# Kernel optimization log

Measured on AMD Instinct MI355X. Metric: run time of the kernel, lower is better.

The kernel has to match this reference:

```python
import jax, jax.numpy as jnp
import numpy as np

R = 200000
PAD = 14            # residue_pad_length (atom14)
ACD, ATD, RCD, RID = 32, 8, 32, 32
N_ATOM_CODES, N_ATOM_TYPES, N_RES_CODES = 38, 6, 21
MAX_SEQ = 1024
OUT_0E, OUT_1E = 128, 32
IN0 = PAD * ACD + PAD * ATD + RCD + RID  # 624 scalar (0e) input channels


def setup_inputs() -> dict:
    key = jax.random.key(0)
    ks = jax.random.split(key, 12)
    counts_np = (4 + (np.arange(R) % 11)).astype(np.int32)  # atoms per residue in [4,14]
    n_atoms = int(counts_np.sum())  # 1,799,991
    residue_index_atomwise = jnp.asarray(np.repeat(np.arange(R, dtype=np.int32), counts_np))
    return {
        "relative_coords": jax.random.normal(ks[0], (n_atoms, 3), dtype=jnp.float32),
        "atom_code_index": jax.random.randint(ks[1], (n_atoms,), 1, N_ATOM_CODES, dtype=jnp.int32),
        "atom_type_index": jax.random.randint(ks[2], (n_atoms,), 1, N_ATOM_TYPES, dtype=jnp.int32),
        "residue_index_atomwise": residue_index_atomwise,
        "counts": jnp.asarray(counts_np),
        "residue_code_index": jax.random.randint(ks[3], (R,), 1, N_RES_CODES, dtype=jnp.int32),
        "residue_sequence_index": jax.random.randint(ks[4], (R,), 0, MAX_SEQ, dtype=jnp.int32),
        "base_coords": jax.random.normal(ks[5], (R, 3), dtype=jnp.float32),
        "atom_code_table": jax.random.normal(ks[6], (N_ATOM_CODES, ACD), dtype=jnp.float32),
        "atom_type_table": jax.random.normal(ks[7], (N_ATOM_TYPES, ATD), dtype=jnp.float32),
        "residue_code_table": jax.random.normal(ks[8], (N_RES_CODES, RCD), dtype=jnp.float32),
        "residue_index_table": jax.random.normal(ks[9], (MAX_SEQ, RID), dtype=jnp.float32),
        "W0": jax.random.normal(ks[10], (IN0, OUT_0E), dtype=jnp.float32),
        "W1": jax.random.normal(ks[11], (PAD, OUT_1E), dtype=jnp.float32),
    }


def _ragged_to_padded(residue_index_atomwise, counts, relative_coords,
                      atom_code_index, atom_type_index):
    # Single O(atoms) scatter replacing the per-residue python loop.
    n_atoms = relative_coords.shape[0]
    nres = counts.shape[0]
    starts = jnp.concatenate([jnp.zeros((1,), counts.dtype), jnp.cumsum(counts)[:-1]])
    pos = jnp.arange(n_atoms, dtype=counts.dtype) - starts[residue_index_atomwise]
    mask = jnp.arange(PAD, dtype=counts.dtype)[None, :] < counts[:, None]  # [R, PAD]
    coords_pad = jnp.zeros((nres, PAD, 3), relative_coords.dtype).at[
        residue_index_atomwise, pos].set(relative_coords)
    codes_pad = jnp.zeros((nres, PAD), jnp.int32).at[residue_index_atomwise, pos].set(atom_code_index)
    types_pad = jnp.zeros((nres, PAD), jnp.int32).at[residue_index_atomwise, pos].set(atom_type_index)
    return coords_pad, codes_pad, types_pad, mask


def reference(relative_coords, atom_code_index, atom_type_index,
              residue_index_atomwise, counts, residue_code_index,
              residue_sequence_index, base_coords,
              atom_code_table, atom_type_table, residue_code_table,
              residue_index_table, W0, W1):
    nres = counts.shape[0]
    coords_pad, codes_pad, types_pad, mask = _ragged_to_padded(
        residue_index_atomwise, counts, relative_coords, atom_code_index, atom_type_index)
    # embedding lookups, masked at padded slots (as in the torch module)
    ac = atom_code_table[codes_pad] * mask[..., None]   # [R, PAD, ACD]
    at = atom_type_table[types_pad] * mask[..., None]   # [R, PAD, ATD]
    rc = residue_code_table[residue_code_index]         # [R, RCD]
    ri = residue_index_table[residue_sequence_index]    # [R, RID]
    scalars = jnp.concatenate(
        [ac.reshape(nres, -1), at.reshape(nres, -1), rc, ri], axis=-1)  # [R, IN0]
    # e3nn o3.Linear: per-irrep-type mixing with 1/sqrt(fan_in) normalization.
    y0 = (scalars @ W0) * (1.0 / jnp.sqrt(jnp.float32(IN0)))            # 0e -> 0e
    y1 = jnp.einsum('rmc,mn->rnc', coords_pad, W1) * (1.0 / jnp.sqrt(jnp.float32(PAD)))  # 1e -> 1e
    features = jnp.concatenate([y0, y1.reshape(nres, -1)], axis=-1)     # [R, 128 + 96]
    return base_coords, features
```

## Files before the change

### kernel.cpp

```cpp
#include <hip/hip_runtime.h>
#include <hip/hip_bf16.h>

#define PAD        14
#define ACD        32
#define ATD        8
#define RCD        32
#define RID        32
#define N_CODES    38
#define N_TYPES    6
#define NCT        (N_CODES * N_TYPES)
#define N_RES      21
#define MAX_SEQ    1024
#define IN0        624
#define OUT0       128
#define OUT1       32
#define FEAT       224

#define NROWS_TCT  (PAD * NCT)
#define ZROW       NROWS_TCT
#define ROW_RC0    (ZROW + 1)
#define ROW_RI0    (ROW_RC0 + N_RES)
#define NROWS_ALL  (ROW_RI0 + MAX_SEQ)

__device__ __constant__ const float NORM0 = 0.04003203845f;
__device__ __constant__ const float NORM1 = 0.26726124191f;

typedef float f32x2 __attribute__((ext_vector_type(2)));

#define SZ_W1N     (PAD * OUT1)

#define T2_SZ_TCT     (PAD * NCT * OUT0)
#define T2_OFF_TCT    0
#define T2_OFF_TRC    (T2_OFF_TCT + T2_SZ_TCT)
#define T2_SZ_TRC     (N_RES * OUT0)
#define T2_OFF_TRI    (T2_OFF_TRC + T2_SZ_TRC)
#define T2_SZ_TRI     (MAX_SEQ * OUT0)
#define T2_OFF_W1N    (T2_OFF_TRI + T2_SZ_TRI)
#define T2_OFF_STARTS (T2_OFF_W1N + SZ_W1N)

__device__ __forceinline__ unsigned short f2bf(float v) {
    __hip_bfloat16 h = __float2bfloat16(v);
    unsigned short u;
    __builtin_memcpy(&u, &h, 2);
    return u;
}
__device__ __forceinline__ float bf_lo(unsigned int d) { return __uint_as_float(d << 16); }
__device__ __forceinline__ float bf_hi(unsigned int d) { return __uint_as_float(d & 0xffff0000u); }

__global__ void build_starts(const int* __restrict__ resIdx, int n_atoms,
                             int* __restrict__ starts,
                             const float* __restrict__ baseIn,
                             float* __restrict__ outBase, int nbase) {
    int i = blockIdx.x * blockDim.x + threadIdx.x;
    if (i < nbase) outBase[i] = baseIn[i];
    if (i >= n_atoms) return;
    int r = resIdx[i];
    if (i == 0 || resIdx[i - 1] != r) starts[r] = i;
}

__global__ void build_tall_meta(
    const float* __restrict__ act, const float* __restrict__ att,
    const float* __restrict__ rct, const float* __restrict__ rit,
    const float* __restrict__ W0, const float* __restrict__ W1,
    __hip_bfloat16* __restrict__ Tall, float* __restrict__ W1n,
    const int* __restrict__ starts, const int* __restrict__ counts,
    const int* __restrict__ codeIdx, const int* __restrict__ typeIdx,
    const float* __restrict__ coords,
    const int* __restrict__ rcIdx, const int* __restrict__ rsIdx,
    unsigned short* __restrict__ meta, int R) {
    int b = blockIdx.x;
    if (b <= NROWS_ALL) {
        int o = threadIdx.x;
        if (o >= OUT0) return;
        float acc = 0.f;
        if (b < NROWS_TCT) {
            int m = b / NCT, ct = b % NCT, c = ct / N_TYPES, t = ct % N_TYPES;
            const float* wc = W0 + (size_t)(m * ACD) * OUT0 + o;
            const float* wt = W0 + (size_t)(PAD * ACD + m * ATD) * OUT0 + o;
#pragma unroll
            for (int j = 0; j < ACD; ++j) acc += act[c * ACD + j] * wc[(size_t)j * OUT0];
#pragma unroll
            for (int j = 0; j < ATD; ++j) acc += att[t * ATD + j] * wt[(size_t)j * OUT0];
            Tall[(size_t)b * OUT0 + o] = __float2bfloat16(acc * NORM0);
        } else if (b == ZROW) {
            Tall[(size_t)b * OUT0 + o] = __float2bfloat16(0.f);
        } else if (b < ROW_RC0 + N_RES) {
            int c = b - ROW_RC0;
            const float* w = W0 + (size_t)(PAD * ACD + PAD * ATD) * OUT0 + o;
#pragma unroll
            for (int j = 0; j < RCD; ++j) acc += rct[c * RCD + j] * w[(size_t)j * OUT0];
            Tall[(size_t)b * OUT0 + o] = __float2bfloat16(acc * NORM0);
        } else if (b < NROWS_ALL) {
            int s = b - ROW_RI0;
            const float* w = W0 + (size_t)(PAD * ACD + PAD * ATD + RCD) * OUT0 + o;
#pragma unroll
            for (int j = 0; j < RID; ++j) acc += rit[s * RID + j] * w[(size_t)j * OUT0];
            Tall[(size_t)b * OUT0 + o] = __float2bfloat16(acc * NORM0);
        } else {
            for (int i = o; i < PAD * OUT1; i += OUT0) W1n[i] = W1[i] * NORM1;
        }
        return;
    }
    int gid = (b - (NROWS_ALL + 1)) * 256 + threadIdx.x;
    int r = gid >> 4, slot = gid & 15;
    if (r >= R) return;
    unsigned short* mp = meta + (size_t)r * 64;
    if (slot < PAD) {
        int cnt = counts[r];
        int row = ZROW;
        float cx = 0.f, cy = 0.f, cz = 0.f;
        if (slot < cnt) {
            int a = starts[r] + slot;
            row = slot * NCT + codeIdx[a] * N_TYPES + typeIdx[a];
            cx = coords[3 * (size_t)a + 0];
            cy = coords[3 * (size_t)a + 1];
            cz = coords[3 * (size_t)a + 2];
        }
        mp[slot]      = (unsigned short)row;
        mp[16 + slot] = f2bf(cx);
        mp[32 + slot] = f2bf(cy);
        mp[48 + slot] = f2bf(cz);
    } else if (slot == 14) {
        mp[14] = (unsigned short)(ROW_RC0 + rcIdx[r]);
    } else {
        mp[15] = (unsigned short)(ROW_RI0 + rsIdx[r]);
    }
}

__global__ __launch_bounds__(256) void main_fast2(
    const int* __restrict__ meta32,
    const unsigned int* __restrict__ Tall,
    const float* __restrict__ W1n,
    float* __restrict__ outFeat, int R) {
    int lane   = threadIdx.x & 63;
    int lane32 = lane & 31;
    int wid    = threadIdx.x >> 6;
    int pr = __builtin_amdgcn_readfirstlane(blockIdx.x * 4 + wid);
    int r0 = pr * 2;
    if (r0 >= R) return;
    bool has1 = (r0 + 1) < R;

    float w14[PAD];
#pragma unroll
    for (int m = 0; m < PAD; ++m) w14[m] = W1n[m * OUT1 + lane32];

    const int* mp = meta32 + (size_t)r0 * 32;
    int md[64];
#pragma unroll
    for (int j = 0; j < 32; ++j) md[j] = mp[j];
    if (has1) {
#pragma unroll
        for (int j = 32; j < 64; ++j) md[j] = mp[j];
    } else {
#pragma unroll
        for (int j = 32; j < 64; ++j) md[j] = 0;
    }

    unsigned int t0[16], t1[16];
#pragma unroll
    for (int k = 0; k < 8; ++k) {
        unsigned int dw = (unsigned int)md[k];
        t0[2 * k]     = Tall[(size_t)(dw & 0xffffu) * 64 + lane];
        t0[2 * k + 1] = Tall[(size_t)(dw >> 16) * 64 + lane];
    }
    if (has1) {
#pragma unroll
        for (int k = 0; k < 8; ++k) {
            unsigned int dw = (unsigned int)md[32 + k];
            t1[2 * k]     = Tall[(size_t)(dw & 0xffffu) * 64 + lane];
            t1[2 * k + 1] = Tall[(size_t)(dw >> 16) * 64 + lane];
        }
    }

    float vx0 = 0.f, vy0 = 0.f, vz0 = 0.f;
    float vx1 = 0.f, vy1 = 0.f, vz1 = 0.f;
#pragma unroll
    for (int m = 0; m < PAD; ++m) {
        int dw = m >> 1;
        unsigned int xd0 = (unsigned int)md[8 + dw];
        unsigned int yd0 = (unsigned int)md[16 + dw];
        unsigned int zd0 = (unsigned int)md[24 + dw];
        float cx0 = (m & 1) ? bf_hi(xd0) : bf_lo(xd0);
        float cy0 = (m & 1) ? bf_hi(yd0) : bf_lo(yd0);
        float cz0 = (m & 1) ? bf_hi(zd0) : bf_lo(zd0);
        vx0 = fmaf(cx0, w14[m], vx0);
        vy0 = fmaf(cy0, w14[m], vy0);
        vz0 = fmaf(cz0, w14[m], vz0);
        unsigned int xd1 = (unsigned int)md[40 + dw];
        unsigned int yd1 = (unsigned int)md[48 + dw];
        unsigned int zd1 = (unsigned int)md[56 + dw];
        float cx1 = (m & 1) ? bf_hi(xd1) : bf_lo(xd1);
        float cy1 = (m & 1) ? bf_hi(yd1) : bf_lo(yd1);
        float cz1 = (m & 1) ? bf_hi(zd1) : bf_lo(zd1);
        vx1 = fmaf(cx1, w14[m], vx1);
        vy1 = fmaf(cy1, w14[m], vy1);
        vz1 = fmaf(cz1, w14[m], vz1);
    }

    float acx0 = 0.f, acy0 = 0.f;
#pragma unroll
    for (int j = 0; j < 16; ++j) { acx0 += bf_lo(t0[j]); acy0 += bf_hi(t0[j]); }

    float* fo0 = outFeat + (size_t)r0 * FEAT;
    f32x2 a0; a0.x = acx0; a0.y = acy0;
    __builtin_nontemporal_store(a0, reinterpret_cast<f32x2*>(fo0) + lane);
    if (lane < 32) {
        float* p = fo0 + OUT0 + 3 * lane32;
        __builtin_nontemporal_store(vx0, p + 0);
        __builtin_nontemporal_store(vy0, p + 1);
        __builtin_nontemporal_store(vz0, p + 2);
    }

    if (has1) {
        float acx1 = 0.f, acy1 = 0.f;
#pragma unroll
        for (int j = 0; j < 16; ++j) { acx1 += bf_lo(t1[j]); acy1 += bf_hi(t1[j]); }
        float* fo1 = fo0 + FEAT;
        f32x2 a1; a1.x = acx1; a1.y = acy1;
        __builtin_nontemporal_store(a1, reinterpret_cast<f32x2*>(fo1) + lane);
        if (lane < 32) {
            float* p = fo1 + OUT0 + 3 * lane32;
            __builtin_nontemporal_store(vx1, p + 0);
            __builtin_nontemporal_store(vy1, p + 1);
            __builtin_nontemporal_store(vz1, p + 2);
        }
    }
}

__global__ void build_tables_t2(const float* __restrict__ act, const float* __restrict__ att,
                                const float* __restrict__ rct, const float* __restrict__ rit,
                                const float* __restrict__ W0, const float* __restrict__ W1,
                                float* __restrict__ Tct, float* __restrict__ Trc,
                                float* __restrict__ Tri, float* __restrict__ W1n) {
    int b = blockIdx.x;
    int o = threadIdx.x;
    float acc = 0.f;
    if (b < PAD * NCT) {
        int m = b / NCT, ct = b % NCT, c = ct / N_TYPES, t = ct % N_TYPES;
        const float* wc = W0 + (size_t)(m * ACD) * OUT0 + o;
        const float* wt = W0 + (size_t)(PAD * ACD + m * ATD) * OUT0 + o;
#pragma unroll
        for (int j = 0; j < ACD; ++j) acc += act[c * ACD + j] * wc[(size_t)j * OUT0];
#pragma unroll
        for (int j = 0; j < ATD; ++j) acc += att[t * ATD + j] * wt[(size_t)j * OUT0];
        Tct[(size_t)b * OUT0 + o] = acc * NORM0;
    } else if (b < PAD * NCT + N_RES) {
        int c = b - PAD * NCT;
        const float* w = W0 + (size_t)(PAD * ACD + PAD * ATD) * OUT0 + o;
#pragma unroll
        for (int j = 0; j < RCD; ++j) acc += rct[c * RCD + j] * w[(size_t)j * OUT0];
        Trc[(size_t)c * OUT0 + o] = acc * NORM0;
    } else if (b < PAD * NCT + N_RES + MAX_SEQ) {
        int s = b - (PAD * NCT + N_RES);
        const float* w = W0 + (size_t)(PAD * ACD + PAD * ATD + RCD) * OUT0 + o;
#pragma unroll
        for (int j = 0; j < RID; ++j) acc += rit[s * RID + j] * w[(size_t)j * OUT0];
        Tri[(size_t)s * OUT0 + o] = acc * NORM0;
    } else {
        for (int i = o; i < PAD * OUT1; i += OUT0) W1n[i] = W1[i] * NORM1;
    }
}

__global__ __launch_bounds__(256) void main_t2(
    const float*  __restrict__ coords, const int* __restrict__ codeIdx,
    const int*    __restrict__ typeIdx, const int* __restrict__ counts,
    const int*    __restrict__ rcIdx, const int* __restrict__ rsIdx,
    const float*  __restrict__ W1n,
    const float*  __restrict__ Tct, const float* __restrict__ Trc,
    const float*  __restrict__ Tri, const int* __restrict__ starts,
    float* __restrict__ outFeat, int R, int n_atoms) {
    int wid  = threadIdx.x >> 6;
    int lane = threadIdx.x & 63;
    int r = __builtin_amdgcn_readfirstlane(blockIdx.x * 4 + wid);
    if (r >= R) return;
    int start = starts[r];
    int cnt   = counts[r];
    int rc    = rcIdx[r];
    int rs    = rsIdx[r];
    int lane32 = lane & 31;
    int ci = 1, ti = 1;
    float crd = 0.f;
    if (lane < PAD) {
        int a = min(start + lane, n_atoms - 1);
        ci = codeIdx[a];
        ti = typeIdx[a];
    }
    if (lane < 3 * PAD) {
        int i3 = min(start * 3 + lane, 3 * n_atoms - 1);
        crd = coords[i3];
    }
    const f32x2* Tct2 = reinterpret_cast<const f32x2*>(Tct);
    const f32x2* Trc2 = reinterpret_cast<const f32x2*>(Trc);
    const f32x2* Tri2 = reinterpret_cast<const f32x2*>(Tri);
    f32x2 a0 = Trc2[(size_t)rc * 64 + lane];
    f32x2 a1 = Tri2[(size_t)rs * 64 + lane];
    int cmax = max(cnt - 1, 0);
    f32x2 t[PAD];
#pragma unroll
    for (int m = 0; m < PAD; ++m) {
        int mm = min(m, cmax);
        int cd = __builtin_amdgcn_readlane(ci, mm);
        int tp = __builtin_amdgcn_readlane(ti, mm);
        t[m] = Tct2[(size_t)(mm * NCT + cd * N_TYPES + tp) * 64 + lane];
    }
    float acx = a0.x + a1.x;
    float acy = a0.y + a1.y;
    float vx = 0.f, vy = 0.f, vz = 0.f;
#pragma unroll
    for (int m = 0; m < PAD; ++m) {
        int mm = min(m, cmax);
        float msk = (m < cnt) ? 1.f : 0.f;
        acx = fmaf(t[m].x, msk, acx);
        acy = fmaf(t[m].y, msk, acy);
        float cx = __uint_as_float(__builtin_amdgcn_readlane(__float_as_uint(crd), 3 * mm + 0));
        float cy = __uint_as_float(__builtin_amdgcn_readlane(__float_as_uint(crd), 3 * mm + 1));
        float cz = __uint_as_float(__builtin_amdgcn_readlane(__float_as_uint(crd), 3 * mm + 2));
        float w  = W1n[m * OUT1 + lane32] * msk;
        vx = fmaf(cx, w, vx);
        vy = fmaf(cy, w, vy);
        vz = fmaf(cz, w, vz);
    }
    float* fo = outFeat + (size_t)r * FEAT;
    f32x2 accv; accv.x = acx; accv.y = acy;
    __builtin_nontemporal_store(accv, reinterpret_cast<f32x2*>(fo) + lane);
    if (lane < 32) {
        float* p = fo + OUT0 + 3 * lane32;
        __builtin_nontemporal_store(vx, p + 0);
        __builtin_nontemporal_store(vy, p + 1);
        __builtin_nontemporal_store(vz, p + 2);
    }
}

__global__ __launch_bounds__(128) void fallback_kernel(
    const float* __restrict__ coords, const int* __restrict__ codeIdx,
    const int* __restrict__ typeIdx, const int* __restrict__ resIdx,
    const int* __restrict__ counts, const int* __restrict__ rcIdx,
    const int* __restrict__ rsIdx, const float* __restrict__ baseIn,
    const float* __restrict__ act, const float* __restrict__ att,
    const float* __restrict__ rct, const float* __restrict__ rit,
    const float* __restrict__ W0, const float* __restrict__ W1,
    float* __restrict__ outBase, float* __restrict__ outFeat, int R, int n_atoms) {
    int r = blockIdx.x, tid = threadIdx.x;
    __shared__ float s[IN0];
    __shared__ int sh_start;
    if (tid == 0) {
        int lo = 0, hi = n_atoms;
        while (lo < hi) { int mid = (lo + hi) >> 1; if (resIdx[mid] < r) lo = mid + 1; else hi = mid; }
        sh_start = lo;
    }
    __syncthreads();
    int start = sh_start, cnt = counts[r];
    for (int j = tid; j < IN0; j += 128) {
        float v = 0.f;
        if (j < PAD * ACD) {
            int m = j >> 5, jj = j & 31;
            if (m < cnt) v = act[codeIdx[start + m] * ACD + jj];
        } else if (j < PAD * ACD + PAD * ATD) {
            int t = j - PAD * ACD; int m = t >> 3, jj = t & 7;
            if (m < cnt) v = att[typeIdx[start + m] * ATD + jj];
        } else if (j < PAD * ACD + PAD * ATD + RCD) {
            v = rct[rcIdx[r] * RCD + (j - PAD * ACD - PAD * ATD)];
        } else {
            v = rit[rsIdx[r] * RID + (j - PAD * ACD - PAD * ATD - RCD)];
        }
        s[j] = v;
    }
    __syncthreads();
    float accv = 0.f;
    for (int j = 0; j < IN0; ++j) accv += s[j] * W0[(size_t)j * OUT0 + tid];
    float* fo = outFeat + (size_t)r * FEAT;
    fo[tid] = accv * NORM0;
    if (tid < 96) {
        int n = tid / 3, c = tid % 3;
        float v = 0.f;
        for (int m = 0; m < cnt; ++m) v += coords[(size_t)(start + m) * 3 + c] * W1[m * OUT1 + n];
        fo[OUT0 + tid] = v * NORM1;
    }
    if (tid < 3) outBase[(size_t)r * 3 + tid] = baseIn[(size_t)r * 3 + tid];
}

extern "C" void kernel_launch(void* const* d_in, const int* in_sizes, int n_in,
                              void* d_out, int out_size, void* d_ws, size_t ws_size,
                              hipStream_t stream) {
    const float* coords = (const float*)d_in[0];
    const int*   codeIdx = (const int*)d_in[1];
    const int*   typeIdx = (const int*)d_in[2];
    const int*   resIdx  = (const int*)d_in[3];
    const int*   counts  = (const int*)d_in[4];
    const int*   rcIdx   = (const int*)d_in[5];
    const int*   rsIdx   = (const int*)d_in[6];
    const float* baseIn  = (const float*)d_in[7];
    const float* act     = (const float*)d_in[8];
    const float* att     = (const float*)d_in[9];
    const float* rct     = (const float*)d_in[10];
    const float* rit     = (const float*)d_in[11];
    const float* W0      = (const float*)d_in[12];
    const float* W1      = (const float*)d_in[13];

    int n_atoms = in_sizes[1];
    int R       = in_sizes[4];

    float* out     = (float*)d_out;
    float* outBase = out;
    float* outFeat = out + (size_t)R * 3;

    size_t tallBytes = (size_t)NROWS_ALL * OUT0 * 2;
    size_t w1nOff    = tallBytes;
    size_t startsOff = w1nOff + (size_t)SZ_W1N * 4;
    size_t metaOff   = (startsOff + (size_t)R * 4 + 255) & ~(size_t)255;
    size_t needFast  = metaOff + (size_t)R * 128;
    size_t needT2    = (size_t)(T2_OFF_STARTS + R) * 4;

    if (ws_size >= needFast) {
        char* wsb = (char*)d_ws;
        __hip_bfloat16* Tall   = (__hip_bfloat16*)wsb;
        unsigned int*   TallU  = (unsigned int*)wsb;
        float*          W1n    = (float*)(wsb + w1nOff);
        int*            starts = (int*)(wsb + startsOff);
        unsigned short* meta   = (unsigned short*)(wsb + metaOff);
        int*            meta32 = (int*)(wsb + metaOff);

        build_starts<<<(n_atoms + 255) / 256, 256, 0, stream>>>(
            resIdx, n_atoms, starts, baseIn, outBase, R * 3);
        int metaBlocks = (int)(((size_t)R * 16 + 255) / 256);
        build_tall_meta<<<(NROWS_ALL + 1) + metaBlocks, 256, 0, stream>>>(
            act, att, rct, rit, W0, W1, Tall, W1n,
            starts, counts, codeIdx, typeIdx, coords, rcIdx, rsIdx, meta, R);
        int pairs = (R + 1) / 2;
        main_fast2<<<(pairs + 3) / 4, 256, 0, stream>>>(
            meta32, TallU, W1n, outFeat, R);
    } else if (ws_size >= needT2) {
        float* ws     = (float*)d_ws;
        float* Tct    = ws + T2_OFF_TCT;
        float* Trc    = ws + T2_OFF_TRC;
        float* Tri    = ws + T2_OFF_TRI;
        float* W1n    = ws + T2_OFF_W1N;
        int*   starts = (int*)(ws + T2_OFF_STARTS);
        build_starts<<<(n_atoms + 255) / 256, 256, 0, stream>>>(
            resIdx, n_atoms, starts, baseIn, outBase, R * 3);
        int nrows = PAD * NCT + N_RES + MAX_SEQ + 1;
        build_tables_t2<<<nrows, OUT0, 0, stream>>>(act, att, rct, rit, W0, W1,
                                                    Tct, Trc, Tri, W1n);
        main_t2<<<(R + 3) / 4, 256, 0, stream>>>(
            coords, codeIdx, typeIdx, counts, rcIdx, rsIdx, W1n,
            Tct, Trc, Tri, starts, outFeat, R, n_atoms);
    } else {
        fallback_kernel<<<R, 128, 0, stream>>>(
            coords, codeIdx, typeIdx, resIdx, counts, rcIdx, rsIdx, baseIn,
            act, att, rct, rit, W0, W1, outBase, outFeat, R, n_atoms);
    }
}
```

Measured before the change: 80.66 us.

## Read fp32 coords directly in main kernel instead of staging bf16 copies in meta

The meta build no longer gathers coordinates and packs them as bf16. It stores each residue's start and count in a smaller 16-dword meta record. The main kernel then loads the contiguous fp32 coordinates per residue straight from the input and masks them by count. This removes a write and read of staged coordinate data and drops the bf16 rounding, at the cost of a wider uniform read of coordinates per wave in the main kernel.

```diff
diff --git a/kernel.cpp b/kernel.cpp
--- a/kernel.cpp
+++ b/kernel.cpp
@@ -29,6 +29,8 @@
 
 #define SZ_W1N     (PAD * OUT1)
 
+#define META_DW    16
+
 #define T2_SZ_TCT     (PAD * NCT * OUT0)
 #define T2_OFF_TCT    0
 #define T2_OFF_TRC    (T2_OFF_TCT + T2_SZ_TCT)
@@ -38,12 +40,6 @@
 #define T2_OFF_W1N    (T2_OFF_TRI + T2_SZ_TRI)
 #define T2_OFF_STARTS (T2_OFF_W1N + SZ_W1N)
 
-__device__ __forceinline__ unsigned short f2bf(float v) {
-    __hip_bfloat16 h = __float2bfloat16(v);
-    unsigned short u;
-    __builtin_memcpy(&u, &h, 2);
-    return u;
-}
 __device__ __forceinline__ float bf_lo(unsigned int d) { return __uint_as_float(d << 16); }
 __device__ __forceinline__ float bf_hi(unsigned int d) { return __uint_as_float(d & 0xffff0000u); }
 
@@ -65,9 +61,8 @@
     __hip_bfloat16* __restrict__ Tall, float* __restrict__ W1n,
     const int* __restrict__ starts, const int* __restrict__ counts,
     const int* __restrict__ codeIdx, const int* __restrict__ typeIdx,
-    const float* __restrict__ coords,
     const int* __restrict__ rcIdx, const int* __restrict__ rsIdx,
-    unsigned short* __restrict__ meta, int R) {
+    unsigned int* __restrict__ meta, int R) {
     int b = blockIdx.x;
     if (b <= NROWS_ALL) {
         int o = threadIdx.x;
@@ -104,34 +99,31 @@
     int gid = (b - (NROWS_ALL + 1)) * 256 + threadIdx.x;
     int r = gid >> 4, slot = gid & 15;
     if (r >= R) return;
-    unsigned short* mp = meta + (size_t)r * 64;
+    unsigned short* mp16 = (unsigned short*)(meta + (size_t)r * META_DW);
+    unsigned int*   mp32 = meta + (size_t)r * META_DW;
     if (slot < PAD) {
         int cnt = counts[r];
         int row = ZROW;
-        float cx = 0.f, cy = 0.f, cz = 0.f;
         if (slot < cnt) {
             int a = starts[r] + slot;
             row = slot * NCT + codeIdx[a] * N_TYPES + typeIdx[a];
-            cx = coords[3 * (size_t)a + 0];
-            cy = coords[3 * (size_t)a + 1];
-            cz = coords[3 * (size_t)a + 2];
-        }
-        mp[slot]      = (unsigned short)row;
-        mp[16 + slot] = f2bf(cx);
-        mp[32 + slot] = f2bf(cy);
-        mp[48 + slot] = f2bf(cz);
+        }
+        mp16[slot] = (unsigned short)row;
     } else if (slot == 14) {
-        mp[14] = (unsigned short)(ROW_RC0 + rcIdx[r]);
+        mp16[14] = (unsigned short)(ROW_RC0 + rcIdx[r]);
+        mp32[8]  = (unsigned int)starts[r];
     } else {
-        mp[15] = (unsigned short)(ROW_RI0 + rsIdx[r]);
+        mp16[15] = (unsigned short)(ROW_RI0 + rsIdx[r]);
+        mp32[9]  = (unsigned int)counts[r];
     }
 }
 
 __global__ __launch_bounds__(256) void main_fast2(
-    const int* __restrict__ meta32,
+    const unsigned int* __restrict__ meta,
     const unsigned int* __restrict__ Tall,
+    const float* __restrict__ coords,
     const float* __restrict__ W1n,
-    float* __restrict__ outFeat, int R) {
+    float* __restrict__ outFeat, int R, int n_atoms) {
     int lane   = threadIdx.x & 63;
     int lane32 = lane & 31;
     int wid    = threadIdx.x >> 6;
@@ -144,54 +136,79 @@
 #pragma unroll
     for (int m = 0; m < PAD; ++m) w14[m] = W1n[m * OUT1 + lane32];
 
-    const int* mp = meta32 + (size_t)r0 * 32;
-    int md[64];
-#pragma unroll
-    for (int j = 0; j < 32; ++j) md[j] = mp[j];
+    const unsigned int* mp = meta + (size_t)r0 * META_DW;
+    unsigned int md[20];
+#pragma unroll
+    for (int j = 0; j < 10; ++j) md[j] = mp[j];
     if (has1) {
 #pragma unroll
-        for (int j = 32; j < 64; ++j) md[j] = mp[j];
+        for (int j = 0; j < 10; ++j) md[10 + j] = mp[META_DW + j];
     } else {
 #pragma unroll
-        for (int j = 32; j < 64; ++j) md[j] = 0;
-    }
+        for (int j = 0; j < 10; ++j) md[10 + j] = 0;
+    }
+    int start0 = (int)md[8],  cnt0 = (int)md[9];
+    int start1 = (int)md[18], cnt1 = (int)md[19];
 
     unsigned int t0[16], t1[16];
 #pragma unroll
     for (int k = 0; k < 8; ++k) {
-        unsigned int dw = (unsigned int)md[k];
+        unsigned int dw = md[k];
         t0[2 * k]     = Tall[(size_t)(dw & 0xffffu) * 64 + lane];
         t0[2 * k + 1] = Tall[(size_t)(dw >> 16) * 64 + lane];
     }
     if (has1) {
 #pragma unroll
         for (int k = 0; k < 8; ++k) {
-            unsigned int dw = (unsigned int)md[32 + k];
+            unsigned int dw = md[10 + k];
             t1[2 * k]     = Tall[(size_t)(dw & 0xffffu) * 64 + lane];
             t1[2 * k + 1] = Tall[(size_t)(dw >> 16) * 64 + lane];
         }
     }
 
+    float cf0[3 * PAD];
+    {
+        bool safe = (start0 + PAD) <= n_atoms;
+        if (safe) {
+            const float* cp = coords + (size_t)start0 * 3;
+#pragma unroll
+            for (int k = 0; k < 3 * PAD; ++k) cf0[k] = cp[k];
+        } else {
+#pragma unroll
+            for (int k = 0; k < 3 * PAD; ++k)
+                cf0[k] = coords[min(start0 * 3 + k, n_atoms * 3 - 1)];
+        }
+    }
+    float cf1[3 * PAD];
+    if (has1) {
+        bool safe = (start1 + PAD) <= n_atoms;
+        if (safe) {
+            const float* cp = coords + (size_t)start1 * 3;
+#pragma unroll
+            for (int k = 0; k < 3 * PAD; ++k) cf1[k] = cp[k];
+        } else {
+#pragma unroll
+            for (int k = 0; k < 3 * PAD; ++k)
+                cf1[k] = coords[min(start1 * 3 + k, n_atoms * 3 - 1)];
+        }
+    } else {
+#pragma unroll
+        for (int k = 0; k < 3 * PAD; ++k) cf1[k] = 0.f;
+    }
+
     float vx0 = 0.f, vy0 = 0.f, vz0 = 0.f;
     float vx1 = 0.f, vy1 = 0.f, vz1 = 0.f;
 #pragma unroll
     for (int m = 0; m < PAD; ++m) {
-        int dw = m >> 1;
-        unsigned int xd0 = (unsigned int)md[8 + dw];
-        unsigned int yd0 = (unsigned int)md[16 + dw];
-        unsigned int zd0 = (unsigned int)md[24 + dw];
-        float cx0 = (m & 1) ? bf_hi(xd0) : bf_lo(xd0);
-        float cy0 = (m & 1) ? bf_hi(yd0) : bf_lo(yd0);
-        float cz0 = (m & 1) ? bf_hi(zd0) : bf_lo(zd0);
+        float cx0 = (m < cnt0) ? cf0[3 * m + 0] : 0.f;
+        float cy0 = (m < cnt0) ? cf0[3 * m + 1] : 0.f;
+        float cz0 = (m < cnt0) ? cf0[3 * m + 2] : 0.f;
         vx0 = fmaf(cx0, w14[m], vx0);
         vy0 = fmaf(cy0, w14[m], vy0);
         vz0 = fmaf(cz0, w14[m], vz0);
-        unsigned int xd1 = (unsigned int)md[40 + dw];
-        unsigned int yd1 = (unsigned int)md[48 + dw];
-        unsigned int zd1 = (unsigned int)md[56 + dw];
-        float cx1 = (m & 1) ? bf_hi(xd1) : bf_lo(xd1);
-        float cy1 = (m & 1) ? bf_hi(yd1) : bf_lo(yd1);
-        float cz1 = (m & 1) ? bf_hi(zd1) : bf_lo(zd1);
+        float cx1 = (m < cnt1) ? cf1[3 * m + 0] : 0.f;
+        float cy1 = (m < cnt1) ? cf1[3 * m + 1] : 0.f;
+        float cz1 = (m < cnt1) ? cf1[3 * m + 2] : 0.f;
         vx1 = fmaf(cx1, w14[m], vx1);
         vy1 = fmaf(cy1, w14[m], vy1);
         vz1 = fmaf(cz1, w14[m], vz1);
@@ -408,7 +425,7 @@
     size_t w1nOff    = tallBytes;
     size_t startsOff = w1nOff + (size_t)SZ_W1N * 4;
     size_t metaOff   = (startsOff + (size_t)R * 4 + 255) & ~(size_t)255;
-    size_t needFast  = metaOff + (size_t)R * 128;
+    size_t needFast  = metaOff + ((size_t)R + 1) * META_DW * 4;
     size_t needT2    = (size_t)(T2_OFF_STARTS + R) * 4;
 
     if (ws_size >= needFast) {
@@ -417,18 +434,17 @@
         unsigned int*   TallU  = (unsigned int*)wsb;
         float*          W1n    = (float*)(wsb + w1nOff);
         int*            starts = (int*)(wsb + startsOff);
-        unsigned short* meta   = (unsigned short*)(wsb + metaOff);
-        int*            meta32 = (int*)(wsb + metaOff);
+        unsigned int*   meta   = (unsigned int*)(wsb + metaOff);
 
         build_starts<<<(n_atoms + 255) / 256, 256, 0, stream>>>(
             resIdx, n_atoms, starts, baseIn, outBase, R * 3);
         int metaBlocks = (int)(((size_t)R * 16 + 255) / 256);
         build_tall_meta<<<(NROWS_ALL + 1) + metaBlocks, 256, 0, stream>>>(
             act, att, rct, rit, W0, W1, Tall, W1n,
-            starts, counts, codeIdx, typeIdx, coords, rcIdx, rsIdx, meta, R);
+            starts, counts, codeIdx, typeIdx, rcIdx, rsIdx, meta, R);
         int pairs = (R + 1) / 2;
         main_fast2<<<(pairs + 3) / 4, 256, 0, stream>>>(
-            meta32, TallU, W1n, outFeat, R);
+            meta, TallU, coords, W1n, outFeat, R, n_atoms);
     } else if (ws_size >= needT2) {
         float* ws     = (float*)d_ws;
         float* Tct    = ws + T2_OFF_TCT;
```

After: 109.3 us. 1.36x slower.
